# Performance work log

Measured on AMD Instinct MI355X. Metric: run time of the kernel, lower is better.

The kernel has to match this reference:

```python
import jax, jax.numpy as jnp
import numpy as np
from jax import lax

EPS = 1e-5

def conv3x3(x, w, b):
    # x: [N,C,H,W], w: [O,I,3,3]
    y = lax.conv_general_dilated(x, w, window_strides=(1, 1), padding='SAME',
                                 dimension_numbers=('NCHW', 'OIHW', 'NCHW'))
    return y + b[None, :, None, None]

def batchnorm(x, gamma, beta):
    # training-mode BN: batch statistics over (N,H,W), biased variance
    mean = x.mean(axis=(0, 2, 3), keepdims=True)
    var = x.var(axis=(0, 2, 3), keepdims=True)
    xn = (x - mean) * lax.rsqrt(var + EPS)
    return xn * gamma[None, :, None, None] + beta[None, :, None, None]

def instance_norm_unbiased(x):
    # per-(sample, channel) mean and unbiased std (torch .std() default ddof=1)
    n = x.shape[2] * x.shape[3]
    m = x.mean(axis=(2, 3), keepdims=True)
    var = ((x - m) ** 2).sum(axis=(2, 3), keepdims=True) / (n - 1)
    return (x - m) / jnp.sqrt(var)

def res_block(x, w, b, g, be):
    # w: [2,64,64,3,3]; b,g,be: [2,64]
    h = x
    for k in range(2):
        h = jax.nn.celu(batchnorm(conv3x3(h, w[k], b[k]), g[k], be[k]))
    return h + x

def setup_inputs() -> dict:
    key = jax.random.key(0)
    ks = jax.random.split(key, 8)
    x = jax.random.normal(ks[0], (8, 3, 256, 256), dtype=jnp.float32)
    w1 = jax.random.normal(ks[1], (64, 6, 3, 3), dtype=jnp.float32) * 0.05
    b1 = jnp.zeros((64,), jnp.float32)
    g1 = jnp.ones((64,), jnp.float32)
    be1 = jnp.zeros((64,), jnp.float32)
    bw = jax.random.normal(ks[2], (3, 2, 64, 64, 3, 3), dtype=jnp.float32) * 0.02
    bb = jnp.zeros((3, 2, 64), jnp.float32)
    bg = jnp.ones((3, 2, 64), jnp.float32)
    bbe = jnp.zeros((3, 2, 64), jnp.float32)
    w2 = jax.random.normal(ks[3], (3, 64, 3, 3), dtype=jnp.float32) * 0.05
    b2 = jnp.zeros((3,), jnp.float32)
    return {"x": x, "w1": w1, "b1": b1, "g1": g1, "be1": be1,
            "bw": bw, "bb": bb, "bg": bg, "bbe": bbe, "w2": w2, "b2": b2}

def reference(x, w1, b1, g1, be1, bw, bb, bg, bbe, w2, b2):
    normalized = instance_norm_unbiased(x)
    inp = jnp.concatenate([x, normalized], axis=1)  # [N,6,H,W]
    out = jax.nn.celu(batchnorm(conv3x3(inp, w1, b1), g1, be1))
    for i in range(3):  # 3 structurally distinct ResBlocks
        out = res_block(out, bw[i], bb[i], bg[i], bbe[i])
    out = jax.nn.celu(conv3x3(out, w2, b2))
    return out + x
```

## Files before the change

kernel.cpp:

```cpp
#include <hip/hip_runtime.h>
#include <cstdint>
#include <cstddef>

#define DEVI __device__ __forceinline__

static constexpr int HW = 65536;
static constexpr float PTOTF = 524288.0f;
static constexpr int NPB = 8192;

typedef __attribute__((ext_vector_type(8))) short bfx8;
typedef __attribute__((ext_vector_type(16))) float fx16;
typedef __attribute__((ext_vector_type(4))) float fx4;

DEVI unsigned short f2bf(float f) {
  unsigned int x = __float_as_uint(f);
  x += 0x7fffu + ((x >> 16) & 1u);
  return (unsigned short)(x >> 16);
}
DEVI float celuf(float v) { return v > 0.0f ? v : expm1f(v); }

DEVI void unpack8(const uint4 u, float* v) {
  v[0] = __uint_as_float(u.x << 16); v[1] = __uint_as_float(u.x & 0xffff0000u);
  v[2] = __uint_as_float(u.y << 16); v[3] = __uint_as_float(u.y & 0xffff0000u);
  v[4] = __uint_as_float(u.z << 16); v[5] = __uint_as_float(u.z & 0xffff0000u);
  v[6] = __uint_as_float(u.w << 16); v[7] = __uint_as_float(u.w & 0xffff0000u);
}

DEVI void gload16(const unsigned short* g, unsigned short* l) {
  __builtin_amdgcn_global_load_lds(
      (const __attribute__((address_space(1))) unsigned int*)g,
      (__attribute__((address_space(3))) unsigned int*)l, 16, 0, 0);
}

DEVI size_t padpx(int n, int h, int w) {
  return ((size_t)n * 258 + (h + 1)) * 258 + (w + 1);
}

__global__ __launch_bounds__(256)
void k_prep(const float* __restrict__ w1, const float* __restrict__ bw,
            const float* __restrict__ w2, float* __restrict__ wt1,
            unsigned short* __restrict__ wtm, unsigned short* __restrict__ wlast,
            unsigned short* a, unsigned short* b, unsigned short* c) {
  int id = blockIdx.x * 256 + threadIdx.x;
  if (id < 24672) {
    const int buf = id / 8224, r = id - buf * 8224;
    const int n = r / 1028, k = r - n * 1028;
    int hp, wp;
    if (k < 258)      { hp = 0;           wp = k; }
    else if (k < 516) { hp = 257;         wp = k - 258; }
    else if (k < 772) { hp = k - 516 + 1; wp = 0; }
    else              { hp = k - 772 + 1; wp = 257; }
    unsigned short* p = (buf == 0 ? a : buf == 1 ? b : c) +
                        (((size_t)n * 258 + hp) * 258 + wp) * 64;
    const uint4 z = {0, 0, 0, 0};
#pragma unroll
    for (int q = 0; q < 8; ++q) ((uint4*)p)[q] = z;
    return;
  }
  id -= 24672;
  if (id < 221184) {
    const int cv = id / 36864, r = id - cv * 36864;
    const int tap = r >> 12, rr = r & 4095, oc = rr >> 6, ic = rr & 63;
    const float v = bw[((size_t)cv * 4096 + oc * 64 + ic) * 9 + tap];
    const int dic = ((((ic >> 3) ^ (oc & 7)) << 3) | (ic & 7));
    wtm[(size_t)cv * 36864 + tap * 4096 + oc * 64 + dic] = f2bf(v);
    return;
  }
  id -= 221184;
  if (id < 4608) {
    const int tap = id / 512, rr = id - tap * 512, ic = rr >> 6, oc = rr & 63;
    wt1[id] = (ic < 6) ? w1[(oc * 6 + ic) * 9 + tap] : 0.0f;
    return;
  }
  id -= 4608;
  if (id < 9216) {
    const int cch = id >> 9, r = id & 511, l = r >> 3, j = r & 7;
    const int oc = l & 15, kg = l >> 4;
    const int tap = cch >> 1, kc = cch & 1;
    const int ic = kc * 32 + kg * 8 + j;
    wlast[id] = (oc < 3) ? f2bf(w2[(oc * 64 + ic) * 9 + tap]) : (unsigned short)0;
  }
}

__global__ __launch_bounds__(256)
void k_inorm(const float* __restrict__ x, float* __restrict__ ms) {
  __shared__ float s1[256], s2[256];
  const int b = blockIdx.x;
  const float4* p = (const float4*)(x + (size_t)b * HW);
  float sum = 0.f, sq = 0.f;
  for (int j = threadIdx.x; j < HW / 4; j += 256) {
    const float4 v = p[j];
    sum += v.x + v.y + v.z + v.w;
    sq  += v.x * v.x + v.y * v.y + v.z * v.z + v.w * v.w;
  }
  s1[threadIdx.x] = sum; s2[threadIdx.x] = sq;
  __syncthreads();
  for (int s = 128; s > 0; s >>= 1) {
    if ((int)threadIdx.x < s) {
      s1[threadIdx.x] += s1[threadIdx.x + s];
      s2[threadIdx.x] += s2[threadIdx.x + s];
    }
    __syncthreads();
  }
  if (threadIdx.x == 0) {
    const float m = s1[0] * (1.0f / HW);
    const float var = (s2[0] - s1[0] * s1[0] * (1.0f / HW)) * (1.0f / (HW - 1));
    ms[2 * b] = m;
    ms[2 * b + 1] = rsqrtf(var);
  }
}

__global__ __launch_bounds__(256)
void k_conv1(const float* __restrict__ x, const float* __restrict__ ms,
             const float* __restrict__ wt, unsigned short* __restrict__ out,
             float* __restrict__ psum, float* __restrict__ psq) {
  __shared__ float in_s[3 * 66 * 9];
  __shared__ float w_s[9 * 8 * 64];
  __shared__ float red0[16][64], red1[16][64];

  const int t = threadIdx.x;
  const int b = blockIdx.x;
  const int n = b >> 10;
  const int h = (b >> 2) & 255;
  const int w0 = (b & 3) << 6;

  const float m0 = ms[6 * n + 0], r0 = ms[6 * n + 1];
  const float m1 = ms[6 * n + 2], r1 = ms[6 * n + 3];
  const float m2 = ms[6 * n + 4], r2 = ms[6 * n + 5];

  const int oc0 = (t & 15) * 4;
  const int px0 = (t >> 4) * 4;
  float acc[4][4] = {{0.f}};

  {
    const float4* wsrc = (const float4*)wt;
    for (int j4 = t; j4 < 1152; j4 += 256) ((float4*)w_s)[j4] = wsrc[j4];
  }
  if (t < 198) {
    const int dh = t / 66, px = t - dh * 66;
    const int gh = h + dh - 1, gw = w0 + px - 1;
    const bool ok = ((unsigned)gh < 256u) && ((unsigned)gw < 256u);
    float v[8];
    if (ok) {
      const float* xp = x + (size_t)n * 3 * HW + gh * 256 + gw;
      const float a0 = xp[0], a1 = xp[HW], a2 = xp[2 * HW];
      v[0] = a0; v[1] = a1; v[2] = a2;
      v[3] = (a0 - m0) * r0; v[4] = (a1 - m1) * r1; v[5] = (a2 - m2) * r2;
      v[6] = 0.f; v[7] = 0.f;
    } else {
#pragma unroll
      for (int q = 0; q < 8; ++q) v[q] = 0.f;
    }
    float* d = &in_s[(dh * 66 + px) * 9];
#pragma unroll
    for (int q = 0; q < 8; ++q) d[q] = v[q];
  }
  __syncthreads();
#pragma unroll
  for (int i = 0; i < 8; ++i) {
    float xv[3][6];
#pragma unroll
    for (int dh = 0; dh < 3; ++dh)
#pragma unroll
      for (int j = 0; j < 6; ++j)
        xv[dh][j] = in_s[(dh * 66 + px0 + j) * 9 + i];
#pragma unroll
    for (int dh = 0; dh < 3; ++dh)
#pragma unroll
      for (int dw = 0; dw < 3; ++dw) {
        const float4 wv = *(const float4*)&w_s[((dh * 3 + dw) * 8 + i) * 64 + oc0];
#pragma unroll
        for (int p = 0; p < 4; ++p) {
          const float xin = xv[dh][p + dw];
          acc[p][0] += xin * wv.x;
          acc[p][1] += xin * wv.y;
          acc[p][2] += xin * wv.z;
          acc[p][3] += xin * wv.w;
        }
      }
  }
  unsigned short* ob = out + (((size_t)n * 258 + (h + 1)) * 258 + (w0 + 1)) * 64;
#pragma unroll
  for (int p = 0; p < 4; ++p) {
    ushort4 o;
    o.x = f2bf(acc[p][0]); o.y = f2bf(acc[p][1]);
    o.z = f2bf(acc[p][2]); o.w = f2bf(acc[p][3]);
    *(ushort4*)(ob + (size_t)(px0 + p) * 64 + oc0) = o;
  }
#pragma unroll
  for (int q = 0; q < 4; ++q) {
    float s = 0.f, qv = 0.f;
#pragma unroll
    for (int p = 0; p < 4; ++p) { s += acc[p][q]; qv += acc[p][q] * acc[p][q]; }
    red0[t >> 4][oc0 + q] = s;
    red1[t >> 4][oc0 + q] = qv;
  }
  __syncthreads();
  if (t < 64) {
    float s = 0.f, qv = 0.f;
#pragma unroll
    for (int g2 = 0; g2 < 16; ++g2) { s += red0[g2][t]; qv += red1[g2][t]; }
    psum[(size_t)t * NPB + b] = s;
    psq[(size_t)t * NPB + b]  = qv;
  }
}

__global__ __launch_bounds__(256)
void k_mconv(const unsigned short* __restrict__ in,
             const unsigned short* __restrict__ wt,
             unsigned short* __restrict__ out) {
  __shared__ __align__(16) unsigned short w_s[36864];
  __shared__ __align__(16) unsigned short ring[10 * 528 * 8];

  const int t = threadIdx.x;
  const int lane = t & 63, wv = t >> 6;
  const int l31 = lane & 31, hi = lane >> 5;
  const int bo = blockIdx.x;
  const int b = (bo & 7) * 64 + (bo >> 3);
  const int n  = b >> 6;
  const int hb = (b >> 2) & 15;
  const int w0 = (b & 3) * 64;

#pragma unroll
  for (int j = 0; j < 18; ++j) {
    const int id = t + j * 256;
    gload16(wt + (size_t)id * 8, w_s + (size_t)id * 8);
  }
  {
    const size_t gb = ((size_t)n * 258 + hb * 16) * 258 + w0;
#pragma unroll
    for (int j = 0; j < 13; ++j) {
      const int id = t + j * 256;
      if (id < 3168) {
        const int r = id / 528, c = id - r * 528;
        const int px = c >> 3;
        const int R = r * 66 + px;
        const int sl = (c & 7) ^ (R & 7);
        gload16(in + (gb + (size_t)r * 258 + px) * 64 + sl * 8,
                ring + (size_t)id * 8);
      }
    }
  }

  for (int k = 0; k < 4; ++k) {
    if (k == 0) { asm volatile("s_waitcnt vmcnt(0)" ::: "memory"); }
    else       { asm volatile("s_waitcnt vmcnt(16)" ::: "memory"); }
    __builtin_amdgcn_sched_barrier(0);
    __builtin_amdgcn_s_barrier();
    __builtin_amdgcn_sched_barrier(0);
    if (k < 3) {
      const int base = 4 * k + 6;
#pragma unroll
      for (int j = 0; j < 9; ++j) {
        const int id = t + j * 256;
        if (id < 2112) {
          const int r = id / 528, c = id - r * 528;
          const int Lr = base + r;
          const int s = (Lr >= 10) ? Lr - 10 : Lr;
          const int px = c >> 3;
          const int R = s * 66 + px;
          const int sl = (c & 7) ^ (R & 7);
          gload16(in + (((size_t)n * 258 + hb * 16 + Lr) * 258 + w0 + px) * 64 + sl * 8,
                  ring + ((size_t)s * 528 + c) * 8);
        }
      }
    }
    __builtin_amdgcn_sched_barrier(0);

    fx16 acc[2][2] = {};
#pragma unroll
    for (int tap = 0; tap < 9; ++tap) {
      const int dh = tap / 3, dw = tap - dh * 3;
      const int Lr = 4 * k + wv + dh;
      const int s = (Lr >= 10) ? Lr - 10 : Lr;
      const int Rbase = s * 66 + dw;
#pragma unroll
      for (int ks = 0; ks < 4; ++ks) {
        bfx8 wf[2], bf[2];
#pragma unroll
        for (int m = 0; m < 2; ++m) {
          const int oc = m * 32 + l31;
          const int slW = (ks * 2 + hi) ^ (oc & 7);
          wf[m] = *(const bfx8*)((const char*)w_s +
                   ((size_t)tap * 4096 + oc * 64) * 2 + (slW << 4));
        }
#pragma unroll
        for (int p = 0; p < 2; ++p) {
          const int R = Rbase + p * 32 + l31;
          const int slA = (ks * 2 + hi) ^ (R & 7);
          bf[p] = *(const bfx8*)((const char*)ring + (size_t)R * 128 + (slA << 4));
        }
#pragma unroll
        for (int m = 0; m < 2; ++m)
#pragma unroll
          for (int p = 0; p < 2; ++p)
            acc[m][p] = __builtin_amdgcn_mfma_f32_32x32x16_bf16(
                wf[m], bf[p], acc[m][p], 0, 0, 0);
      }
    }

    const int orow = hb * 16 + 4 * k + wv + 1;
    const size_t obase = (((size_t)n * 258 + orow) * 258 + (w0 + 1)) * 64;
#pragma unroll
    for (int m = 0; m < 2; ++m)
#pragma unroll
      for (int p = 0; p < 2; ++p) {
        const int px = p * 32 + l31;
#pragma unroll
        for (int q = 0; q < 4; ++q) {
          const int ocb = m * 32 + q * 8 + 4 * hi;
          ushort4 o;
          o.x = f2bf(acc[m][p][q * 4 + 0]);
          o.y = f2bf(acc[m][p][q * 4 + 1]);
          o.z = f2bf(acc[m][p][q * 4 + 2]);
          o.w = f2bf(acc[m][p][q * 4 + 3]);
          *(ushort4*)(out + obase + (size_t)px * 64 + ocb) = o;
        }
      }
  }
}

__global__ __launch_bounds__(256)
void k_bnstats(const unsigned short* __restrict__ y, float* __restrict__ psum,
               float* __restrict__ psq) {
  __shared__ float r0[32][64], r1[32][64];
  const int b = blockIdx.x, t = threadIdx.x;
  const int c8 = (t & 7) * 8, pg = t >> 3;
  float sv[8] = {0.f}, qv[8] = {0.f};
#pragma unroll
  for (int j = 0; j < 16; ++j) {
    const int px = b * 512 + pg * 16 + j;
    const int n = px >> 16, hh = (px >> 8) & 255, ww = px & 255;
    float v[8];
    unpack8(*(const uint4*)(y + padpx(n, hh, ww) * 64 + c8), v);
#pragma unroll
    for (int q = 0; q < 8; ++q) { sv[q] += v[q]; qv[q] += v[q] * v[q]; }
  }
#pragma unroll
  for (int q = 0; q < 8; ++q) { r0[pg][c8 + q] = sv[q]; r1[pg][c8 + q] = qv[q]; }
  __syncthreads();
  if (t < 64) {
    float s = 0.f, q2 = 0.f;
#pragma unroll
    for (int g = 0; g < 32; ++g) { s += r0[g][t]; q2 += r1[g][t]; }
    psum[(size_t)t * NPB + b] = s;
    psq [(size_t)t * NPB + b] = q2;
  }
}

__global__ __launch_bounds__(256)
void k_bnfin(const float* __restrict__ psum, const float* __restrict__ psq,
             const float* __restrict__ g, const float* __restrict__ be,
             float* __restrict__ bnp, int nb) {
  __shared__ float s1[256], s2[256];
  const int c = blockIdx.x;
  const int t = threadIdx.x;
  float s = 0.f, q = 0.f;
  for (int j = t; j < nb; j += 256) {
    s += psum[(size_t)c * NPB + j];
    q += psq[(size_t)c * NPB + j];
  }
  s1[t] = s; s2[t] = q;
  __syncthreads();
  for (int st = 128; st > 0; st >>= 1) {
    if (t < st) { s1[t] += s1[t + st]; s2[t] += s2[t + st]; }
    __syncthreads();
  }
  if (t == 0) {
    const float m = s1[0] / PTOTF;
    const float var = s2[0] / PTOTF - m * m;
    const float sc = g[c] * rsqrtf(var + 1e-5f);
    bnp[c] = sc;
    bnp[64 + c] = be[c] - m * sc;
  }
}

template<int RES>
__global__ __launch_bounds__(256)
void k_apply(const unsigned short* __restrict__ y, const float* __restrict__ bnp,
             unsigned short* __restrict__ a) {
  const size_t gid = (size_t)blockIdx.x * 256 + threadIdx.x;
  const int px = (int)(gid >> 3);
  const int c0 = ((int)gid & 7) * 8;
  const int n = px >> 16, hh = (px >> 8) & 255, ww = px & 255;
  const size_t i = padpx(n, hh, ww) * 64 + c0;
  float v[8];
  unpack8(*(const uint4*)(y + i), v);
  const float4 sa = *(const float4*)(bnp + c0);
  const float4 sb = *(const float4*)(bnp + c0 + 4);
  const float4 ha = *(const float4*)(bnp + 64 + c0);
  const float4 hb = *(const float4*)(bnp + 64 + c0 + 4);
  const float sc[8] = {sa.x, sa.y, sa.z, sa.w, sb.x, sb.y, sb.z, sb.w};
  const float sh[8] = {ha.x, ha.y, ha.z, ha.w, hb.x, hb.y, hb.z, hb.w};
  float r[8];
#pragma unroll
  for (int q = 0; q < 8; ++q) r[q] = celuf(v[q] * sc[q] + sh[q]);
  if (RES) {
    float av[8];
    unpack8(*(const uint4*)(a + i), av);
#pragma unroll
    for (int q = 0; q < 8; ++q) r[q] += av[q];
  }
  uint4 o;
  o.x = (unsigned)f2bf(r[0]) | ((unsigned)f2bf(r[1]) << 16);
  o.y = (unsigned)f2bf(r[2]) | ((unsigned)f2bf(r[3]) << 16);
  o.z = (unsigned)f2bf(r[4]) | ((unsigned)f2bf(r[5]) << 16);
  o.w = (unsigned)f2bf(r[6]) | ((unsigned)f2bf(r[7]) << 16);
  *(uint4*)(a + i) = o;
}

__global__ __launch_bounds__(256, 2)
void k_last(const unsigned short* __restrict__ a, const float* __restrict__ x,
            const unsigned short* __restrict__ wl, const float* __restrict__ b2,
            float* __restrict__ outp) {
  __shared__ __align__(16) unsigned short a_s[3168 * 8];

  const int t = threadIdx.x;
  const int lane = t & 63, wv = t >> 6;
  int b = blockIdx.x;
  b = (b & 7) * 256 + (b >> 3);
  const int n  = b >> 8;
  const int h0 = ((b >> 2) & 63) * 4;
  const int w0 = (b & 3) * 64;

  const size_t ibase = ((size_t)n * 258 + h0) * 258 + w0;
  for (int seg = wv; seg < 54; seg += 4) {
    const int r = seg / 9;
    const int p = seg - r * 9;
    const int c = p * 64 + lane;
    const int px = c >> 3;
    const int R = r * 66 + px;
    const int sl = (c & 7) ^ (R & 7);
    if (c < 528)
      gload16(a + (ibase + (size_t)r * 258 + px) * 64 + sl * 8,
              a_s + (size_t)(r * 528 + p * 64) * 8);
  }
  __syncthreads();

  const int col = lane & 15, kg = lane >> 4;
  const float bz0 = b2[0], bz1 = b2[1], bz2 = b2[2];
#pragma unroll
  for (int ti = 0; ti < 4; ++ti) {
    fx4 acc = {};
#pragma unroll
    for (int tap = 0; tap < 9; ++tap) {
      const int dh = tap / 3, dw = tap - dh * 3;
      const int px = ti * 16 + col + dw;
      const int R = (wv + dh) * 66 + px;
#pragma unroll
      for (int kc = 0; kc < 2; ++kc) {
        const int s = kc * 4 + kg;
        const bfx8 bf = *(const bfx8*)((const char*)a_s +
            (size_t)R * 128 + ((s ^ (R & 7)) << 4));
        const bfx8 af = *(const bfx8*)(wl + ((size_t)(tap * 2 + kc) * 64 + lane) * 8);
        acc = __builtin_amdgcn_mfma_f32_16x16x32_bf16(af, bf, acc, 0, 0, 0);
      }
    }
    if (kg == 0) {
      const int h = h0 + wv;
      const size_t ob = (size_t)n * 3 * HW + ((size_t)h << 8) + w0 + ti * 16 + col;
      outp[ob]          = celuf(acc[0] + bz0) + x[ob];
      outp[ob + HW]     = celuf(acc[1] + bz1) + x[ob + HW];
      outp[ob + 2 * HW] = celuf(acc[2] + bz2) + x[ob + 2 * HW];
    }
  }
}

extern "C" void kernel_launch(void* const* d_in, const int* in_sizes, int n_in,
                              void* d_out, int out_size, void* d_ws, size_t ws_size,
                              hipStream_t stream) {
  const float* x   = (const float*)d_in[0];
  const float* w1  = (const float*)d_in[1];
  const float* g1  = (const float*)d_in[3];
  const float* be1 = (const float*)d_in[4];
  const float* bw  = (const float*)d_in[5];
  const float* bg  = (const float*)d_in[7];
  const float* bbe = (const float*)d_in[8];
  const float* w2  = (const float*)d_in[9];
  const float* b2  = (const float*)d_in[10];
  float* out = (float*)d_out;

  const size_t PADBUF = (size_t)8 * 258 * 258 * 64 * 2;
  size_t off = 0;
  auto alloc = [&](size_t bytes) {
    size_t cur = off;
    off += (bytes + 255) & ~(size_t)255;
    return cur;
  };
  const size_t oA   = alloc(PADBUF);
  const size_t oB   = alloc(PADBUF);
  const size_t oC   = alloc(PADBUF);
  const size_t oW1  = alloc(4608 * 4);
  const size_t oWM  = alloc((size_t)6 * 36864 * 2);
  const size_t oWL  = alloc(9216 * 2);
  const size_t oMS  = alloc(48 * 4);
  const size_t oBNP = alloc(7 * 128 * 4);
  const size_t oPS  = alloc((size_t)64 * NPB * 4);
  const size_t oPQ  = alloc((size_t)64 * NPB * 4);
  if (off > ws_size) return;

  char* wsb = (char*)d_ws;
  unsigned short* bufA = (unsigned short*)(wsb + oA);
  unsigned short* bufB = (unsigned short*)(wsb + oB);
  unsigned short* bufC = (unsigned short*)(wsb + oC);
  float* wt1 = (float*)(wsb + oW1);
  unsigned short* wtm = (unsigned short*)(wsb + oWM);
  unsigned short* wlast = (unsigned short*)(wsb + oWL);
  float* ms  = (float*)(wsb + oMS);
  float* bnp = (float*)(wsb + oBNP);
  float* psum = (float*)(wsb + oPS);
  float* psq  = (float*)(wsb + oPQ);

  k_prep<<<1015, 256, 0, stream>>>(w1, bw, w2, wt1, wtm, wlast, bufA, bufB, bufC);
  k_inorm<<<24, 256, 0, stream>>>(x, ms);

  k_conv1<<<8192, 256, 0, stream>>>(x, ms, wt1, bufB, psum, psq);
  k_bnfin<<<64, 256, 0, stream>>>(psum, psq, g1, be1, bnp, 8192);
  k_apply<0><<<16384, 256, 0, stream>>>(bufB, bnp, bufA);

  for (int i = 0; i < 3; ++i) {
    const int s1 = 1 + 2 * i, s2 = 2 + 2 * i;
    k_mconv<<<512, 256, 0, stream>>>(bufA, wtm + (size_t)(2 * i) * 36864, bufB);
    k_bnstats<<<1024, 256, 0, stream>>>(bufB, psum, psq);
    k_bnfin<<<64, 256, 0, stream>>>(psum, psq, bg + (size_t)(2 * i) * 64,
        bbe + (size_t)(2 * i) * 64, bnp + (size_t)s1 * 128, 1024);
    k_apply<0><<<16384, 256, 0, stream>>>(bufB, bnp + (size_t)s1 * 128, bufC);
    k_mconv<<<512, 256, 0, stream>>>(bufC, wtm + (size_t)(2 * i + 1) * 36864, bufB);
    k_bnstats<<<1024, 256, 0, stream>>>(bufB, psum, psq);
    k_bnfin<<<64, 256, 0, stream>>>(psum, psq, bg + (size_t)(2 * i + 1) * 64,
        bbe + (size_t)(2 * i + 1) * 64, bnp + (size_t)s2 * 128, 1024);
    k_apply<1><<<16384, 256, 0, stream>>>(bufB, bnp + (size_t)s2 * 128, bufA);
  }

  k_last<<<2048, 256, 0, stream>>>(bufA, x, wlast, b2, out);
}
```

Baseline: 750.9 us.

## Fuse BN statistics into MFMA convs and move first conv to bf16 MFMA

The first 6→64 conv, which was scalar fp32 FMA, now runs on bf16 MFMA with 4 rows per block, using repacked bf16 weights. The per-channel sum and sum-of-squares reduction is fused into the epilogue of both the first conv and the residual conv kernels. This removes the six separate k_bnstats passes that re-read each conv output from memory. In exchange, the first conv's inputs and weights are rounded to bf16, and the conv epilogues gain shuffle reductions and extra registers.

Result: faster. 688.1 us (-8.4%).

```diff
diff --git a/kernel.cpp b/kernel.cpp
--- a/kernel.cpp
+++ b/kernel.cpp
@@ -38,7 +38,7 @@
 
 __global__ __launch_bounds__(256)
 void k_prep(const float* __restrict__ w1, const float* __restrict__ bw,
-            const float* __restrict__ w2, float* __restrict__ wt1,
+            const float* __restrict__ w2, unsigned short* __restrict__ wc1,
             unsigned short* __restrict__ wtm, unsigned short* __restrict__ wlast,
             unsigned short* a, unsigned short* b, unsigned short* c) {
   int id = blockIdx.x * 256 + threadIdx.x;
@@ -67,12 +67,16 @@
     return;
   }
   id -= 221184;
-  if (id < 4608) {
-    const int tap = id / 512, rr = id - tap * 512, ic = rr >> 6, oc = rr & 63;
-    wt1[id] = (ic < 6) ? w1[(oc * 6 + ic) * 9 + tap] : 0.0f;
+  if (id < 5120) {
+    const int cch = id >> 10, rr = id & 1023;
+    const int m = rr >> 9, l = (rr >> 3) & 63, j = rr & 7;
+    const int oc = m * 32 + (l & 31);
+    const int tap = 2 * cch + (l >> 5);
+    wc1[id] = (tap < 9 && j < 6) ? f2bf(w1[(oc * 6 + j) * 9 + tap])
+                                 : (unsigned short)0;
     return;
   }
-  id -= 4608;
+  id -= 5120;
   if (id < 9216) {
     const int cch = id >> 9, r = id & 511, l = r >> 3, j = r & 7;
     const int oc = l & 15, kg = l >> 4;
@@ -112,105 +116,124 @@
 
 __global__ __launch_bounds__(256)
 void k_conv1(const float* __restrict__ x, const float* __restrict__ ms,
-             const float* __restrict__ wt, unsigned short* __restrict__ out,
+             const unsigned short* __restrict__ wc1, unsigned short* __restrict__ out,
              float* __restrict__ psum, float* __restrict__ psq) {
-  __shared__ float in_s[3 * 66 * 9];
-  __shared__ float w_s[9 * 8 * 64];
-  __shared__ float red0[16][64], red1[16][64];
+  __shared__ __align__(16) unsigned short in_s[6 * 66 * 8];
+  __shared__ float s_red[2][4][64];
 
   const int t = threadIdx.x;
+  const int lane = t & 63, wv = t >> 6;
+  const int l31 = lane & 31, hi = lane >> 5;
   const int b = blockIdx.x;
-  const int n = b >> 10;
-  const int h = (b >> 2) & 255;
-  const int w0 = (b & 3) << 6;
+  const int n = b >> 8;
+  const int h0 = ((b >> 2) & 63) * 4;
+  const int w0 = (b & 3) * 64;
 
   const float m0 = ms[6 * n + 0], r0 = ms[6 * n + 1];
   const float m1 = ms[6 * n + 2], r1 = ms[6 * n + 3];
   const float m2 = ms[6 * n + 4], r2 = ms[6 * n + 5];
 
-  const int oc0 = (t & 15) * 4;
-  const int px0 = (t >> 4) * 4;
-  float acc[4][4] = {{0.f}};
-
-  {
-    const float4* wsrc = (const float4*)wt;
-    for (int j4 = t; j4 < 1152; j4 += 256) ((float4*)w_s)[j4] = wsrc[j4];
-  }
-  if (t < 198) {
-    const int dh = t / 66, px = t - dh * 66;
-    const int gh = h + dh - 1, gw = w0 + px - 1;
-    const bool ok = ((unsigned)gh < 256u) && ((unsigned)gw < 256u);
-    float v[8];
-    if (ok) {
+  for (int id = t; id < 396; id += 256) {
+    const int r = id / 66, px = id - r * 66;
+    const int gh = h0 + r - 1, gw = w0 + px - 1;
+    uint4 u = {0, 0, 0, 0};
+    if (((unsigned)gh < 256u) && ((unsigned)gw < 256u)) {
       const float* xp = x + (size_t)n * 3 * HW + gh * 256 + gw;
       const float a0 = xp[0], a1 = xp[HW], a2 = xp[2 * HW];
-      v[0] = a0; v[1] = a1; v[2] = a2;
-      v[3] = (a0 - m0) * r0; v[4] = (a1 - m1) * r1; v[5] = (a2 - m2) * r2;
-      v[6] = 0.f; v[7] = 0.f;
-    } else {
-#pragma unroll
-      for (int q = 0; q < 8; ++q) v[q] = 0.f;
-    }
-    float* d = &in_s[(dh * 66 + px) * 9];
-#pragma unroll
-    for (int q = 0; q < 8; ++q) d[q] = v[q];
+      const float n0 = (a0 - m0) * r0, n1 = (a1 - m1) * r1, n2 = (a2 - m2) * r2;
+      u.x = (unsigned)f2bf(a0) | ((unsigned)f2bf(a1) << 16);
+      u.y = (unsigned)f2bf(a2) | ((unsigned)f2bf(n0) << 16);
+      u.z = (unsigned)f2bf(n1) | ((unsigned)f2bf(n2) << 16);
+    }
+    *(uint4*)(in_s + (size_t)id * 8) = u;
   }
   __syncthreads();
-#pragma unroll
-  for (int i = 0; i < 8; ++i) {
-    float xv[3][6];
-#pragma unroll
-    for (int dh = 0; dh < 3; ++dh)
-#pragma unroll
-      for (int j = 0; j < 6; ++j)
-        xv[dh][j] = in_s[(dh * 66 + px0 + j) * 9 + i];
-#pragma unroll
-    for (int dh = 0; dh < 3; ++dh)
-#pragma unroll
-      for (int dw = 0; dw < 3; ++dw) {
-        const float4 wv = *(const float4*)&w_s[((dh * 3 + dw) * 8 + i) * 64 + oc0];
-#pragma unroll
-        for (int p = 0; p < 4; ++p) {
-          const float xin = xv[dh][p + dw];
-          acc[p][0] += xin * wv.x;
-          acc[p][1] += xin * wv.y;
-          acc[p][2] += xin * wv.z;
-          acc[p][3] += xin * wv.w;
-        }
-      }
-  }
-  unsigned short* ob = out + (((size_t)n * 258 + (h + 1)) * 258 + (w0 + 1)) * 64;
-#pragma unroll
-  for (int p = 0; p < 4; ++p) {
-    ushort4 o;
-    o.x = f2bf(acc[p][0]); o.y = f2bf(acc[p][1]);
-    o.z = f2bf(acc[p][2]); o.w = f2bf(acc[p][3]);
-    *(ushort4*)(ob + (size_t)(px0 + p) * 64 + oc0) = o;
-  }
-#pragma unroll
-  for (int q = 0; q < 4; ++q) {
-    float s = 0.f, qv = 0.f;
-#pragma unroll
-    for (int p = 0; p < 4; ++p) { s += acc[p][q]; qv += acc[p][q] * acc[p][q]; }
-    red0[t >> 4][oc0 + q] = s;
-    red1[t >> 4][oc0 + q] = qv;
+
+  fx16 acc[2][2] = {};
+#pragma unroll
+  for (int c = 0; c < 5; ++c) {
+    bfx8 af[2];
+#pragma unroll
+    for (int m = 0; m < 2; ++m)
+      af[m] = *(const bfx8*)(wc1 + ((size_t)(c * 2 + m) * 64 + lane) * 8);
+    const int tap = 2 * c + hi;
+    const int dh = (tap < 9) ? tap / 3 : 0;
+    const int dw = (tap < 9) ? (tap - (tap / 3) * 3) : 0;
+    bfx8 bf[2];
+#pragma unroll
+    for (int p = 0; p < 2; ++p) {
+      const int px = p * 32 + l31 + dw;
+      bf[p] = *(const bfx8*)(in_s + ((size_t)(wv + dh) * 66 + px) * 8);
+    }
+#pragma unroll
+    for (int m = 0; m < 2; ++m)
+#pragma unroll
+      for (int p = 0; p < 2; ++p)
+        acc[m][p] = __builtin_amdgcn_mfma_f32_32x32x16_bf16(
+            af[m], bf[p], acc[m][p], 0, 0, 0);
+  }
+
+  const size_t obase = (((size_t)n * 258 + (h0 + wv + 1)) * 258 + (w0 + 1)) * 64;
+  float sv[2][16], qv[2][16];
+#pragma unroll
+  for (int m = 0; m < 2; ++m) {
+#pragma unroll
+    for (int p = 0; p < 2; ++p) {
+      const int px = p * 32 + l31;
+#pragma unroll
+      for (int q = 0; q < 4; ++q) {
+        const int ocb = m * 32 + q * 8 + 4 * hi;
+        ushort4 o;
+        o.x = f2bf(acc[m][p][q * 4 + 0]);
+        o.y = f2bf(acc[m][p][q * 4 + 1]);
+        o.z = f2bf(acc[m][p][q * 4 + 2]);
+        o.w = f2bf(acc[m][p][q * 4 + 3]);
+        *(ushort4*)(out + obase + (size_t)px * 64 + ocb) = o;
+      }
+    }
+#pragma unroll
+    for (int r = 0; r < 16; ++r) {
+      const float a0 = acc[m][0][r], a1 = acc[m][1][r];
+      sv[m][r] = a0 + a1;
+      qv[m][r] = a0 * a0 + a1 * a1;
+    }
+  }
+#pragma unroll
+  for (int st = 1; st <= 16; st <<= 1)
+#pragma unroll
+    for (int m = 0; m < 2; ++m)
+#pragma unroll
+      for (int r = 0; r < 16; ++r) {
+        sv[m][r] += __shfl_xor(sv[m][r], st);
+        qv[m][r] += __shfl_xor(qv[m][r], st);
+      }
+  if (l31 == 0) {
+#pragma unroll
+    for (int m = 0; m < 2; ++m)
+#pragma unroll
+      for (int r = 0; r < 16; ++r) {
+        const int oc = m * 32 + (r & 3) + 8 * (r >> 2) + 4 * hi;
+        s_red[0][wv][oc] = sv[m][r];
+        s_red[1][wv][oc] = qv[m][r];
+      }
   }
   __syncthreads();
   if (t < 64) {
-    float s = 0.f, qv = 0.f;
-#pragma unroll
-    for (int g2 = 0; g2 < 16; ++g2) { s += red0[g2][t]; qv += red1[g2][t]; }
-    psum[(size_t)t * NPB + b] = s;
-    psq[(size_t)t * NPB + b]  = qv;
+    psum[(size_t)t * NPB + b] = s_red[0][0][t] + s_red[0][1][t] +
+                                s_red[0][2][t] + s_red[0][3][t];
+    psq [(size_t)t * NPB + b] = s_red[1][0][t] + s_red[1][1][t] +
+                                s_red[1][2][t] + s_red[1][3][t];
   }
 }
 
 __global__ __launch_bounds__(256)
 void k_mconv(const unsigned short* __restrict__ in,
              const unsigned short* __restrict__ wt,
-             unsigned short* __restrict__ out) {
+             unsigned short* __restrict__ out,
+             float* __restrict__ psum, float* __restrict__ psq) {
   __shared__ __align__(16) unsigned short w_s[36864];
   __shared__ __align__(16) unsigned short ring[10 * 528 * 8];
+  __shared__ float s_red[2][4][64];
 
   const int t = threadIdx.x;
   const int lane = t & 63, wv = t >> 6;
@@ -241,6 +264,8 @@
       }
     }
   }
+
+  float sv[2][16] = {{0.f}}, qv[2][16] = {{0.f}};
 
   for (int k = 0; k < 4; ++k) {
     if (k == 0) { asm volatile("s_waitcnt vmcnt(0)" ::: "memory"); }
@@ -302,7 +327,7 @@
     const int orow = hb * 16 + 4 * k + wv + 1;
     const size_t obase = (((size_t)n * 258 + orow) * 258 + (w0 + 1)) * 64;
 #pragma unroll
-    for (int m = 0; m < 2; ++m)
+    for (int m = 0; m < 2; ++m) {
 #pragma unroll
       for (int p = 0; p < 2; ++p) {
         const int px = p * 32 + l31;
@@ -317,34 +342,40 @@
           *(ushort4*)(out + obase + (size_t)px * 64 + ocb) = o;
         }
       }
-  }
-}
-
-__global__ __launch_bounds__(256)
-void k_bnstats(const unsigned short* __restrict__ y, float* __restrict__ psum,
-               float* __restrict__ psq) {
-  __shared__ float r0[32][64], r1[32][64];
-  const int b = blockIdx.x, t = threadIdx.x;
-  const int c8 = (t & 7) * 8, pg = t >> 3;
-  float sv[8] = {0.f}, qv[8] = {0.f};
-#pragma unroll
-  for (int j = 0; j < 16; ++j) {
-    const int px = b * 512 + pg * 16 + j;
-    const int n = px >> 16, hh = (px >> 8) & 255, ww = px & 255;
-    float v[8];
-    unpack8(*(const uint4*)(y + padpx(n, hh, ww) * 64 + c8), v);
-#pragma unroll
-    for (int q = 0; q < 8; ++q) { sv[q] += v[q]; qv[q] += v[q] * v[q]; }
-  }
-#pragma unroll
-  for (int q = 0; q < 8; ++q) { r0[pg][c8 + q] = sv[q]; r1[pg][c8 + q] = qv[q]; }
+#pragma unroll
+      for (int r = 0; r < 16; ++r) {
+        const float a0 = acc[m][0][r], a1 = acc[m][1][r];
+        sv[m][r] += a0 + a1;
+        qv[m][r] += a0 * a0 + a1 * a1;
+      }
+    }
+  }
+
+#pragma unroll
+  for (int st = 1; st <= 16; st <<= 1)
+#pragma unroll
+    for (int m = 0; m < 2; ++m)
+#pragma unroll
+      for (int r = 0; r < 16; ++r) {
+        sv[m][r] += __shfl_xor(sv[m][r], st);
+        qv[m][r] += __shfl_xor(qv[m][r], st);
+      }
+  if (l31 == 0) {
+#pragma unroll
+    for (int m = 0; m < 2; ++m)
+#pragma unroll
+      for (int r = 0; r < 16; ++r) {
+        const int oc = m * 32 + (r & 3) + 8 * (r >> 2) + 4 * hi;
+        s_red[0][wv][oc] = sv[m][r];
+        s_red[1][wv][oc] = qv[m][r];
+      }
+  }
   __syncthreads();
   if (t < 64) {
-    float s = 0.f, q2 = 0.f;
-#pragma unroll
-    for (int g = 0; g < 32; ++g) { s += r0[g][t]; q2 += r1[g][t]; }
-    psum[(size_t)t * NPB + b] = s;
-    psq [(size_t)t * NPB + b] = q2;
+    psum[(size_t)t * NPB + bo] = s_red[0][0][t] + s_red[0][1][t] +
+                                 s_red[0][2][t] + s_red[0][3][t];
+    psq [(size_t)t * NPB + bo] = s_red[1][0][t] + s_red[1][1][t] +
+                                 s_red[1][2][t] + s_red[1][3][t];
   }
 }
 
@@ -490,7 +521,7 @@
   const size_t oA   = alloc(PADBUF);
   const size_t oB   = alloc(PADBUF);
   const size_t oC   = alloc(PADBUF);
-  const size_t oW1  = alloc(4608 * 4);
+  const size_t oW1  = alloc(5120 * 2);
   const size_t oWM  = alloc((size_t)6 * 36864 * 2);
   const size_t oWL  = alloc(9216 * 2);
   const size_t oMS  = alloc(48 * 4);
@@ -503,7 +534,7 @@
   unsigned short* bufA = (unsigned short*)(wsb + oA);
   unsigned short* bufB = (unsigned short*)(wsb + oB);
   unsigned short* bufC = (unsigned short*)(wsb + oC);
-  float* wt1 = (float*)(wsb + oW1);
+  unsigned short* wc1 = (unsigned short*)(wsb + oW1);
   unsigned short* wtm = (unsigned short*)(wsb + oWM);
   unsigned short* wlast = (unsigned short*)(wsb + oWL);
   float* ms  = (float*)(wsb + oMS);
@@ -511,24 +542,24 @@
   float* psum = (float*)(wsb + oPS);
   float* psq  = (float*)(wsb + oPQ);
 
-  k_prep<<<1015, 256, 0, stream>>>(w1, bw, w2, wt1, wtm, wlast, bufA, bufB, bufC);
+  k_prep<<<1017, 256, 0, stream>>>(w1, bw, w2, wc1, wtm, wlast, bufA, bufB, bufC);
   k_inorm<<<24, 256, 0, stream>>>(x, ms);
 
-  k_conv1<<<8192, 256, 0, stream>>>(x, ms, wt1, bufB, psum, psq);
-  k_bnfin<<<64, 256, 0, stream>>>(psum, psq, g1, be1, bnp, 8192);
+  k_conv1<<<2048, 256, 0, stream>>>(x, ms, wc1, bufB, psum, psq);
+  k_bnfin<<<64, 256, 0, stream>>>(psum, psq, g1, be1, bnp, 2048);
   k_apply<0><<<16384, 256, 0, stream>>>(bufB, bnp, bufA);
 
   for (int i = 0; i < 3; ++i) {
     const int s1 = 1 + 2 * i, s2 = 2 + 2 * i;
-    k_mconv<<<512, 256, 0, stream>>>(bufA, wtm + (size_t)(2 * i) * 36864, bufB);
-    k_bnstats<<<1024, 256, 0, stream>>>(bufB, psum, psq);
+    k_mconv<<<512, 256, 0, stream>>>(bufA, wtm + (size_t)(2 * i) * 36864,
+                                     bufB, psum, psq);
     k_bnfin<<<64, 256, 0, stream>>>(psum, psq, bg + (size_t)(2 * i) * 64,
-        bbe + (size_t)(2 * i) * 64, bnp + (size_t)s1 * 128, 1024);
+        bbe + (size_t)(2 * i) * 64, bnp + (size_t)s1 * 128, 512);
     k_apply<0><<<16384, 256, 0, stream>>>(bufB, bnp + (size_t)s1 * 128, bufC);
-    k_mconv<<<512, 256, 0, stream>>>(bufC, wtm + (size_t)(2 * i + 1) * 36864, bufB);
-    k_bnstats<<<1024, 256, 0, stream>>>(bufB, psum, psq);
+    k_mconv<<<512, 256, 0, stream>>>(bufC, wtm + (size_t)(2 * i + 1) * 36864,
+                                     bufB, psum, psq);
     k_bnfin<<<64, 256, 0, stream>>>(psum, psq, bg + (size_t)(2 * i + 1) * 64,
-        bbe + (size_t)(2 * i + 1) * 64, bnp + (size_t)s2 * 128, 1024);
+        bbe + (size_t)(2 * i + 1) * 64, bnp + (size_t)s2 * 128, 512);
     k_apply<1><<<16384, 256, 0, stream>>>(bufB, bnp + (size_t)s2 * 128, bufA);
   }
 
```
